# Performance work log

Measured on AMD Instinct MI355X. Metric: run time of the kernel, lower is better.

Reference implementation:

```python
import jax, jax.numpy as jnp
import numpy as np

EMA_BETA = 0.9
NUM_HEADS = 16

def causal_prefix_ema(x, beta):
    # x: [b, t, d]; s_t = beta*s_{t-1} + (1-beta)*x_t, s_{-1}=0
    def step(s, xt):
        s = beta * s + (1.0 - beta) * xt
        return s, s
    s0 = jnp.zeros_like(x[:, 0, :])
    _, ys = jax.lax.scan(step, s0, jnp.swapaxes(x, 0, 1))  # [t, b, d]
    return jnp.swapaxes(ys, 0, 1)

def setup_inputs() -> dict:
    key = jax.random.key(0)
    ks = jax.random.split(key, 9)
    b, t, d = 2, 1024, 2048
    sc = lambda fan_in: 1.0 / np.sqrt(fan_in)
    return {
        "x": jax.random.normal(ks[0], (b, t, d), jnp.float32),
        "l3_memory": jax.random.normal(ks[1], (b, 1, d), jnp.float32),
        "wq": jax.random.normal(ks[2], (d, d), jnp.float32) * sc(d),
        "wk": jax.random.normal(ks[3], (d, d), jnp.float32) * sc(d),
        "wv": jax.random.normal(ks[4], (d, d), jnp.float32) * sc(d),
        "wo": jax.random.normal(ks[5], (d, d), jnp.float32) * sc(d),
        "rw1": jax.random.normal(ks[6], (d // 2, d), jnp.float32) * sc(d),
        "rb1": jnp.zeros((d // 2,), jnp.float32),
        "rw2": jax.random.normal(ks[7], (3, d // 2), jnp.float32) * sc(d // 2),
        "rb2": jnp.zeros((3,), jnp.float32),
    }

def reference(x, l3_memory, wq, wk, wv, wo, rw1, rb1, rw2, rb2):
    b, t, d = x.shape
    h = NUM_HEADS
    dh = d // h
    scale = 1.0 / np.sqrt(dh)

    q = x @ wq.T                                   # [b,t,d]
    l1 = x
    l2 = causal_prefix_ema(x, EMA_BETA)            # [b,t,d]
    l3 = jnp.broadcast_to(l3_memory, (b, t, d))    # repeat retrieval memory to length t

    # router: MLP(Q) -> softmax over 3 levels
    hdn = jax.nn.silu(q @ rw1.T + rb1)
    lam = jax.nn.softmax(hdn @ rw2.T + rb2, axis=-1)  # [b,t,3]

    fused = lam[..., 0:1] * l1 + lam[..., 1:2] * l2 + lam[..., 2:3] * l3

    def heads(y):
        return jnp.swapaxes(y.reshape(b, t, h, dh), 1, 2)  # [b,h,t,dh]

    qh = heads(q)
    kh = heads(fused @ wk.T)
    vh = heads(fused @ wv.T)

    scores = jnp.einsum("bhqd,bhkd->bhqk", qh, kh) * scale
    causal = jnp.tril(jnp.ones((t, t), bool))
    scores = jnp.where(causal, scores, jnp.finfo(scores.dtype).min)
    attn = jax.nn.softmax(scores, axis=-1)
    out = jnp.einsum("bhqk,bhkd->bhqd", attn, vh)

    out = jnp.swapaxes(out, 1, 2).reshape(b, t, d) @ wo.T
    return (out, kh, vh, lam)
```

## Files before the change

### kernel.cpp

```cpp
#include <hip/hip_runtime.h>
#include <hip/hip_bf16.h>
#include <math.h>

#define B_  2
#define T_  1024
#define D_  2048
#define H_  16
#define DH_ 128
#define M_  2048
#define DR_ 1024

typedef __attribute__((ext_vector_type(8))) short short8;
typedef __attribute__((ext_vector_type(4))) short sh4;
typedef __attribute__((ext_vector_type(4))) float f32x4;

__device__ __forceinline__ void gld16(const __hip_bfloat16* g, __hip_bfloat16* l) {
  __builtin_amdgcn_global_load_lds(
      (const __attribute__((address_space(1))) unsigned int*)g,
      (__attribute__((address_space(3))) unsigned int*)l, 16, 0, 0);
}

template<int BM, int CMODE, bool SILU>
__global__ __launch_bounds__(256)
void gemm_mfma(const __hip_bfloat16* __restrict__ A,
               const __hip_bfloat16* __restrict__ Bm,
               const float* __restrict__ bias,
               float* __restrict__ C, __hip_bfloat16* __restrict__ Cb,
               float* __restrict__ C2, __hip_bfloat16* __restrict__ Cb2,
               int M, int N, int K)
{
  constexpr int NI = BM / 32;
  constexpr int AC = BM / 64;
  __shared__ __hip_bfloat16 As[2][2][BM * 32];
  __shared__ __hip_bfloat16 Bs[2][2][128 * 32];
  const int tid  = threadIdx.x;
  const int wave = tid >> 6;
  const int lane = tid & 63;
  const int m0 = blockIdx.y * BM;
  const int n0 = blockIdx.x * 128;
  const int wm = (wave >> 1) * (BM / 2);
  const int wn = (wave & 1) * 64;

  const int srow = lane >> 2;
  const int scol = (lane & 3) * 8;
  const __hip_bfloat16* Ag = A  + (size_t)(m0 + wave * (BM / 4) + srow) * K + scol;
  const __hip_bfloat16* Bg = Bm + (size_t)(n0 + wave * 32 + srow) * K + scol;

  const int fr = lane & 15;
  const int fk = (lane >> 4) * 8;

  f32x4 acc[NI][4];
  #pragma unroll
  for (int i = 0; i < NI; ++i)
    #pragma unroll
    for (int j = 0; j < 4; ++j) acc[i][j] = (f32x4)0.f;

  auto stage = [&](int bf, int k0) {
    #pragma unroll
    for (int h = 0; h < 2; ++h) {
      #pragma unroll
      for (int c = 0; c < AC; ++c)
        gld16(Ag + k0 + h * 32 + (size_t)(c * 16) * K,
              &As[bf][h][(wave * (BM / 4) + c * 16) * 32]);
      #pragma unroll
      for (int c = 0; c < 2; ++c)
        gld16(Bg + k0 + h * 32 + (size_t)(c * 16) * K,
              &Bs[bf][h][(wave * 32 + c * 16) * 32]);
    }
  };

  stage(0, 0);
  __syncthreads();
  int cur = 0;
  for (int k0 = 0; k0 < K; k0 += 64) {
    if (k0 + 64 < K) stage(cur ^ 1, k0 + 64);
    #pragma unroll
    for (int h = 0; h < 2; ++h) {
      short8 af[NI], bfr[4];
      #pragma unroll
      for (int i = 0; i < NI; ++i)
        af[i]  = *(const short8*)&As[cur][h][(wm + i * 16 + fr) * 32 + fk];
      #pragma unroll
      for (int j = 0; j < 4; ++j)
        bfr[j] = *(const short8*)&Bs[cur][h][(wn + j * 16 + fr) * 32 + fk];
      #pragma unroll
      for (int i = 0; i < NI; ++i)
        #pragma unroll
        for (int j = 0; j < 4; ++j)
          acc[i][j] = __builtin_amdgcn_mfma_f32_16x16x32_bf16(af[i], bfr[j], acc[i][j], 0, 0, 0);
    }
    __syncthreads();
    cur ^= 1;
  }

  #pragma unroll
  for (int i = 0; i < NI; ++i) {
    #pragma unroll
    for (int j = 0; j < 4; ++j) {
      const int row0 = m0 + wm + i * 16 + (lane >> 4) * 4;
      const int col  = n0 + wn + j * 16 + (lane & 15);
      float vr[4];
      #pragma unroll
      for (int r = 0; r < 4; ++r) {
        float v = acc[i][j][r];
        if (bias) v += bias[col];
        if (SILU) v = v / (1.f + __expf(-v));
        vr[r] = v;
      }
      if (CMODE == 0) {
        #pragma unroll
        for (int r = 0; r < 4; ++r) C[(size_t)(row0 + r) * N + col] = vr[r];
      } else if (CMODE == 1) {
        #pragma unroll
        for (int r = 0; r < 4; ++r) Cb[(size_t)(row0 + r) * N + col] = __float2bfloat16(vr[r]);
      } else {
        const int bb = row0 >> 10, t0v = row0 & 1023;
        if (col < D_) {
          const int hh = col >> 7, dd = col & 127;
          #pragma unroll
          for (int r = 0; r < 4; ++r) {
            const size_t idx = (((size_t)(bb * H_ + hh)) * T_ + t0v + r) * DH_ + dd;
            C[idx] = vr[r];
            Cb[idx] = __float2bfloat16(vr[r]);
          }
        } else {
          const int c2 = col - D_;
          const int hh = c2 >> 7, dd = c2 & 127;
          #pragma unroll
          for (int r = 0; r < 4; ++r)
            C2[(((size_t)(bb * H_ + hh)) * T_ + t0v + r) * DH_ + dd] = vr[r];
          __hip_bfloat16 tmp[4];
          #pragma unroll
          for (int r = 0; r < 4; ++r) tmp[r] = __float2bfloat16(vr[r]);
          *(sh4*)(Cb2 + (((size_t)(bb * H_ + hh)) * DH_ + dd) * T_ + t0v) = *(const sh4*)tmp;
        }
      }
    }
  }
}

__global__ __launch_bounds__(256)
void cvt6(const float* __restrict__ s0, const float* __restrict__ s1,
          const float* __restrict__ s2, const float* __restrict__ s3,
          const float* __restrict__ s4, const float* __restrict__ s5,
          __hip_bfloat16* d0, __hip_bfloat16* d1, __hip_bfloat16* d2,
          __hip_bfloat16* d3, __hip_bfloat16* d4, __hip_bfloat16* d5,
          int n0, int n1, int n2, int n3, int n4, int n5)
{
  const float* s; __hip_bfloat16* d; int n;
  switch (blockIdx.y) {
    case 0: s = s0; d = d0; n = n0; break;
    case 1: s = s1; d = d1; n = n1; break;
    case 2: s = s2; d = d2; n = n2; break;
    case 3: s = s3; d = d3; n = n3; break;
    case 4: s = s4; d = d4; n = n4; break;
    default: s = s5; d = d5; n = n5; break;
  }
  const int i = (blockIdx.x * 256 + threadIdx.x) * 4;
  if (i < n) {
    float4 v = *(const float4*)(s + i);
    d[i + 0] = __float2bfloat16(v.x);
    d[i + 1] = __float2bfloat16(v.y);
    d[i + 2] = __float2bfloat16(v.z);
    d[i + 3] = __float2bfloat16(v.w);
  }
}

__global__ __launch_bounds__(256)
void ema_scan(const float* __restrict__ x, float* __restrict__ l2)
{
  const int b  = blockIdx.z;
  const int t0 = blockIdx.y * 64;
  const int d  = blockIdx.x * 256 + threadIdx.x;
  const float* xp = x  + (size_t)b * T_ * D_ + d;
  float*       lp = l2 + (size_t)b * T_ * D_ + d;
  float s = 0.f;
  #pragma unroll 4
  for (int t = t0; t < t0 + 64; ++t) {
    s = 0.9f * s + 0.1f * xp[(size_t)t * D_];
    lp[(size_t)t * D_] = s;
  }
}

__global__ __launch_bounds__(256)
void ema_carry(const float* __restrict__ l2loc, float* __restrict__ carry)
{
  const int i = blockIdx.x * 256 + threadIdx.x;
  const int b = i >> 11, d = i & 2047;
  const float A = 1.1790184577738583e-3f;
  float c = 0.f;
  carry[((size_t)b * 16 + 0) * D_ + d] = 0.f;
  for (int ch = 1; ch < 16; ++ch) {
    const float lf = l2loc[((size_t)b * T_ + ch * 64 - 1) * D_ + d];
    c = lf + A * c;
    carry[((size_t)b * 16 + ch) * D_ + d] = c;
  }
}

__global__ __launch_bounds__(256)
void router_kernel(const float* __restrict__ hdn, const float* __restrict__ rw2,
                   const float* __restrict__ rb2, float* __restrict__ lam)
{
  const int lane = threadIdx.x & 63;
  const int w    = threadIdx.x >> 6;
  const int m    = blockIdx.x * 4 + w;
  const float* hp = hdn + (size_t)m * DR_;
  float s0 = 0.f, s1 = 0.f, s2 = 0.f;
  for (int k = lane * 4; k < DR_; k += 256) {
    float4 h4 = *(const float4*)(hp + k);
    float4 w0 = *(const float4*)(rw2 + k);
    float4 w1 = *(const float4*)(rw2 + DR_ + k);
    float4 w2 = *(const float4*)(rw2 + 2 * DR_ + k);
    s0 += h4.x * w0.x + h4.y * w0.y + h4.z * w0.z + h4.w * w0.w;
    s1 += h4.x * w1.x + h4.y * w1.y + h4.z * w1.z + h4.w * w1.w;
    s2 += h4.x * w2.x + h4.y * w2.y + h4.z * w2.z + h4.w * w2.w;
  }
  #pragma unroll
  for (int off = 32; off > 0; off >>= 1) {
    s0 += __shfl_down(s0, off);
    s1 += __shfl_down(s1, off);
    s2 += __shfl_down(s2, off);
  }
  if (lane == 0) {
    s0 += rb2[0]; s1 += rb2[1]; s2 += rb2[2];
    float mx = fmaxf(s0, fmaxf(s1, s2));
    float e0 = __expf(s0 - mx), e1 = __expf(s1 - mx), e2 = __expf(s2 - mx);
    float inv = 1.f / (e0 + e1 + e2);
    lam[(size_t)m * 3 + 0] = e0 * inv;
    lam[(size_t)m * 3 + 1] = e1 * inv;
    lam[(size_t)m * 3 + 2] = e2 * inv;
  }
}

__global__ __launch_bounds__(256)
void fuse_bf16(const float* __restrict__ x, const float* __restrict__ l2,
               const float* __restrict__ l3m, const float* __restrict__ lam,
               const float* __restrict__ carry, __hip_bfloat16* __restrict__ fb)
{
  const int i4 = blockIdx.x * 256 + threadIdx.x;
  const int m  = i4 >> 9;
  const int c  = (i4 & 511) << 2;
  const int b  = m >> 10;
  const int t  = m & 1023;
  const int ch = t >> 6, off = t & 63;
  const float p = __expf((float)(off + 1) * -0.105360515657f);
  const float w0 = lam[m * 3 + 0], w1 = lam[m * 3 + 1], w2 = lam[m * 3 + 2];
  const float4 xv = *(const float4*)(x   + (size_t)m * D_ + c);
  const float4 ev = *(const float4*)(l2  + (size_t)m * D_ + c);
  const float4 gv = *(const float4*)(l3m + (size_t)b * D_ + c);
  const float4 cv = *(const float4*)(carry + ((size_t)b * 16 + ch) * D_ + c);
  __hip_bfloat16* o = fb + (size_t)m * D_ + c;
  o[0] = __float2bfloat16(w0 * xv.x + w1 * (ev.x + p * cv.x) + w2 * gv.x);
  o[1] = __float2bfloat16(w0 * xv.y + w1 * (ev.y + p * cv.y) + w2 * gv.y);
  o[2] = __float2bfloat16(w0 * xv.z + w1 * (ev.z + p * cv.z) + w2 * gv.z);
  o[3] = __float2bfloat16(w0 * xv.w + w1 * (ev.w + p * cv.w) + w2 * gv.w);
}

__global__ __launch_bounds__(256)
void flash_mfma(const __hip_bfloat16* __restrict__ qg,
                const __hip_bfloat16* __restrict__ kg,
                const __hip_bfloat16* __restrict__ vg,
                __hip_bfloat16* __restrict__ og)
{
  __shared__ __hip_bfloat16 Ks[64 * 136];
  __shared__ __hip_bfloat16 Vt[128 * 72];
  __shared__ __hip_bfloat16 Ps[64 * 72];
  const int tid  = threadIdx.x;
  const int wave = tid >> 6, lane = tid & 63;
  const int L    = blockIdx.x;
  const int halfg = L >> 8, idx = L & 255;
  const int bh = (idx >> 4) | (halfg << 4);
  const int qt = halfg ? (15 - (idx & 15)) : (idx & 15);
  const int b = bh >> 4, h = bh & 15;
  const int q0 = qt * 64;
  const int lo = lane & 15, hi = lane >> 4;

  short8 aq[4];
  {
    const __hip_bfloat16* qsrc = qg + (size_t)(b * T_ + q0 + wave * 16 + lo) * D_ + h * DH_;
    #pragma unroll
    for (int kk = 0; kk < 4; ++kk)
      aq[kk] = *(const short8*)(qsrc + kk * 32 + hi * 8);
  }

  f32x4 oacc[8];
  #pragma unroll
  for (int i = 0; i < 8; ++i) oacc[i] = (f32x4)0.f;
  float mrow[4] = {-INFINITY, -INFINITY, -INFINITY, -INFINITY};
  float lrow[4] = {0.f, 0.f, 0.f, 0.f};

  const __hip_bfloat16* kbp = kg + (size_t)bh * T_ * DH_;
  const __hip_bfloat16* vbp = vg + (size_t)bh * DH_ * T_;
  const float scale = 0.08838834764831845f;

  short8 kreg[4], vreg[4];
  auto load_tile = [&](int k0) {
    #pragma unroll
    for (int i = 0; i < 4; ++i) {
      const int ci = tid + 256 * i;
      const int r = ci >> 4, j = ci & 15;
      kreg[i] = *(const short8*)(kbp + (size_t)(k0 + r) * DH_ + j * 8);
      const int dd = ci >> 3, j2 = ci & 7;
      vreg[i] = *(const short8*)(vbp + (size_t)dd * T_ + k0 + j2 * 8);
    }
  };

  load_tile(0);
  for (int kt = 0; kt <= qt; ++kt) {
    #pragma unroll
    for (int i = 0; i < 4; ++i) {
      const int ci = tid + 256 * i;
      const int r = ci >> 4, j = ci & 15;
      *(short8*)&Ks[r * 136 + j * 8] = kreg[i];
      const int dd = ci >> 3, j2 = ci & 7;
      *(short8*)&Vt[dd * 72 + j2 * 8] = vreg[i];
    }
    __syncthreads();
    if (kt < qt) load_tile((kt + 1) * 64);

    f32x4 sc[4];
    __builtin_amdgcn_s_setprio(1);
    #pragma unroll
    for (int nt = 0; nt < 4; ++nt) {
      sc[nt] = (f32x4)0.f;
      #pragma unroll
      for (int kk = 0; kk < 4; ++kk) {
        short8 bk = *(const short8*)&Ks[(nt * 16 + lo) * 136 + kk * 32 + hi * 8];
        sc[nt] = __builtin_amdgcn_mfma_f32_16x16x32_bf16(aq[kk], bk, sc[nt], 0, 0, 0);
      }
    }
    __builtin_amdgcn_s_setprio(0);
    #pragma unroll
    for (int nt = 0; nt < 4; ++nt)
      #pragma unroll
      for (int r = 0; r < 4; ++r) sc[nt][r] *= scale;
    if (kt == qt) {
      const int qrow = q0 + wave * 16 + hi * 4;
      #pragma unroll
      for (int nt = 0; nt < 4; ++nt) {
        const int key = qt * 64 + nt * 16 + lo;
        #pragma unroll
        for (int r = 0; r < 4; ++r)
          if (key > qrow + r) sc[nt][r] = -1e30f;
      }
    }
    float alpha[4];
    #pragma unroll
    for (int r = 0; r < 4; ++r) {
      float mx = fmaxf(fmaxf(sc[0][r], sc[1][r]), fmaxf(sc[2][r], sc[3][r]));
      mx = fmaxf(mx, __shfl_xor(mx, 1));
      mx = fmaxf(mx, __shfl_xor(mx, 2));
      mx = fmaxf(mx, __shfl_xor(mx, 4));
      mx = fmaxf(mx, __shfl_xor(mx, 8));
      const float nm = fmaxf(mrow[r], mx);
      alpha[r] = __expf(mrow[r] - nm);
      mrow[r] = nm;
      float ls = 0.f;
      #pragma unroll
      for (int nt = 0; nt < 4; ++nt) {
        float p = __expf(sc[nt][r] - nm);
        sc[nt][r] = p;
        ls += p;
      }
      ls += __shfl_xor(ls, 1);
      ls += __shfl_xor(ls, 2);
      ls += __shfl_xor(ls, 4);
      ls += __shfl_xor(ls, 8);
      lrow[r] = lrow[r] * alpha[r] + ls;
    }
    #pragma unroll
    for (int nt = 0; nt < 4; ++nt)
      #pragma unroll
      for (int r = 0; r < 4; ++r)
        Ps[(wave * 16 + hi * 4 + r) * 72 + nt * 16 + lo] = __float2bfloat16(sc[nt][r]);
    #pragma unroll
    for (int n2 = 0; n2 < 8; ++n2)
      #pragma unroll
      for (int r = 0; r < 4; ++r) oacc[n2][r] *= alpha[r];
    short8 ap[2];
    #pragma unroll
    for (int k2 = 0; k2 < 2; ++k2)
      ap[k2] = *(const short8*)&Ps[(wave * 16 + lo) * 72 + k2 * 32 + hi * 8];
    __builtin_amdgcn_s_setprio(1);
    #pragma unroll
    for (int n2 = 0; n2 < 8; ++n2) {
      #pragma unroll
      for (int k2 = 0; k2 < 2; ++k2) {
        short8 bv = *(const short8*)&Vt[(n2 * 16 + lo) * 72 + k2 * 32 + hi * 8];
        oacc[n2] = __builtin_amdgcn_mfma_f32_16x16x32_bf16(ap[k2], bv, oacc[n2], 0, 0, 0);
      }
    }
    __builtin_amdgcn_s_setprio(0);
    __syncthreads();
  }

  float inv[4];
  #pragma unroll
  for (int r = 0; r < 4; ++r) inv[r] = 1.f / lrow[r];
  __hip_bfloat16* od = og + (size_t)(b * T_ + q0 + wave * 16 + hi * 4) * D_ + h * DH_;
  #pragma unroll
  for (int n2 = 0; n2 < 8; ++n2)
    #pragma unroll
    for (int r = 0; r < 4; ++r)
      od[(size_t)r * D_ + n2 * 16 + lo] = __float2bfloat16(oacc[n2][r] * inv[r]);
}

extern "C" void kernel_launch(void* const* d_in, const int* in_sizes, int n_in,
                              void* d_out, int out_size, void* d_ws, size_t ws_size,
                              hipStream_t stream)
{
  const float* x   = (const float*)d_in[0];
  const float* l3m = (const float*)d_in[1];
  const float* wq  = (const float*)d_in[2];
  const float* wk  = (const float*)d_in[3];
  const float* wv  = (const float*)d_in[4];
  const float* wo  = (const float*)d_in[5];
  const float* rw1 = (const float*)d_in[6];
  const float* rb1 = (const float*)d_in[7];
  const float* rw2 = (const float*)d_in[8];
  const float* rb2 = (const float*)d_in[9];

  float* out = (float*)d_out;
  float* kh  = out + 4194304;
  float* vh  = out + 8388608;
  float* lam = out + 12582912;

  char* wsb = (char*)d_ws;
  float*          l2_f32 = (float*)(wsb);
  float*          hdn    = (float*)(wsb + (16u << 20));
  __hip_bfloat16* wkb    = (__hip_bfloat16*)(wsb + (24u << 20));
  __hip_bfloat16* wvb    = (__hip_bfloat16*)(wsb + (32u << 20));
  __hip_bfloat16* wob    = (__hip_bfloat16*)(wsb + (40u << 20));
  __hip_bfloat16* fusedb = (__hip_bfloat16*)(wsb + (48u << 20));
  __hip_bfloat16* attnb  = (__hip_bfloat16*)(wsb + (56u << 20));
  __hip_bfloat16* khb    = (__hip_bfloat16*)(wsb + (64u << 20));
  __hip_bfloat16* vtb    = (__hip_bfloat16*)(wsb + (72u << 20));
  float*          carry  = (float*)attnb;
  __hip_bfloat16* wqb  = (__hip_bfloat16*)kh;
  __hip_bfloat16* rw1b = (__hip_bfloat16*)kh + 4194304;
  __hip_bfloat16* xb   = (__hip_bfloat16*)vh;
  __hip_bfloat16* qb   = (__hip_bfloat16*)out;

  dim3 blk(256);

  cvt6<<<dim3(4096, 6), blk, 0, stream>>>(x, wq, wk, wv, wo, rw1,
                                          xb, wqb, wkb, wvb, wob, rw1b,
                                          M_ * D_, D_ * D_, D_ * D_, D_ * D_, D_ * D_, DR_ * D_);
  ema_scan<<<dim3(8, 16, 2), blk, 0, stream>>>(x, l2_f32);
  ema_carry<<<dim3(16), blk, 0, stream>>>(l2_f32, carry);
  gemm_mfma<64, 1, false><<<dim3(16, 32), blk, 0, stream>>>(xb, wqb, nullptr, nullptr, qb, nullptr, nullptr, M_, D_, D_);
  gemm_mfma<64, 0, true><<<dim3(8, 32), blk, 0, stream>>>(qb, rw1b, rb1, hdn, nullptr, nullptr, nullptr, M_, DR_, D_);
  router_kernel<<<dim3(512), blk, 0, stream>>>(hdn, rw2, rb2, lam);
  fuse_bf16<<<dim3(4096), blk, 0, stream>>>(x, l2_f32, l3m, lam, carry, fusedb);
  gemm_mfma<128, 4, false><<<dim3(32, 16), blk, 0, stream>>>(fusedb, wkb, nullptr, kh, khb, vh, vtb, M_, 2 * D_, D_);
  flash_mfma<<<dim3(512), blk, 0, stream>>>(qb, khb, vtb, attnb);
  gemm_mfma<64, 0, false><<<dim3(16, 32), blk, 0, stream>>>(attnb, wob, nullptr, out, nullptr, nullptr, nullptr, M_, D_, D_);
}
```

Measured before the change: 345.9 us.

## Use 4-stage LDS ring with explicit vmcnt waits in GEMM mainloop

Replaces the double-buffered 64-wide K step with a 4-buffer ring of 32-wide K tiles, prefetching three tiles ahead. Explicit s_waitcnt vmcnt counts and a raw s_barrier replace __syncthreads, so in-flight global-to-LDS loads can overlap MFMA work. It also raises wave priority around the MFMA block. The hand-coded vmcnt values depend on the exact number of loads issued per stage, and one barrier per iteration with the ring spacing relies on subtle reuse safety.

Measured after the change: 366.8 us. +6.1%, slower.

```diff
diff --git a/kernel.cpp b/kernel.cpp
--- a/kernel.cpp
+++ b/kernel.cpp
@@ -20,6 +20,8 @@
       (__attribute__((address_space(3))) unsigned int*)l, 16, 0, 0);
 }
 
+#define WAITV(n) asm volatile("s_waitcnt vmcnt(" #n ")" ::: "memory")
+
 template<int BM, int CMODE, bool SILU>
 __global__ __launch_bounds__(256)
 void gemm_mfma(const __hip_bfloat16* __restrict__ A,
@@ -31,8 +33,8 @@
 {
   constexpr int NI = BM / 32;
   constexpr int AC = BM / 64;
-  __shared__ __hip_bfloat16 As[2][2][BM * 32];
-  __shared__ __hip_bfloat16 Bs[2][2][128 * 32];
+  __shared__ __hip_bfloat16 As[4][BM * 32];
+  __shared__ __hip_bfloat16 Bs[4][128 * 32];
   const int tid  = threadIdx.x;
   const int wave = tid >> 6;
   const int lane = tid & 63;
@@ -57,40 +59,50 @@
 
   auto stage = [&](int bf, int k0) {
     #pragma unroll
-    for (int h = 0; h < 2; ++h) {
-      #pragma unroll
-      for (int c = 0; c < AC; ++c)
-        gld16(Ag + k0 + h * 32 + (size_t)(c * 16) * K,
-              &As[bf][h][(wave * (BM / 4) + c * 16) * 32]);
-      #pragma unroll
-      for (int c = 0; c < 2; ++c)
-        gld16(Bg + k0 + h * 32 + (size_t)(c * 16) * K,
-              &Bs[bf][h][(wave * 32 + c * 16) * 32]);
-    }
+    for (int c = 0; c < AC; ++c)
+      gld16(Ag + k0 + (size_t)(c * 16) * K,
+            &As[bf][(wave * (BM / 4) + c * 16) * 32]);
+    #pragma unroll
+    for (int c = 0; c < 2; ++c)
+      gld16(Bg + k0 + (size_t)(c * 16) * K,
+            &Bs[bf][(wave * 32 + c * 16) * 32]);
   };
 
+  const int NT = K >> 5;
   stage(0, 0);
-  __syncthreads();
-  int cur = 0;
-  for (int k0 = 0; k0 < K; k0 += 64) {
-    if (k0 + 64 < K) stage(cur ^ 1, k0 + 64);
-    #pragma unroll
-    for (int h = 0; h < 2; ++h) {
-      short8 af[NI], bfr[4];
-      #pragma unroll
-      for (int i = 0; i < NI; ++i)
-        af[i]  = *(const short8*)&As[cur][h][(wm + i * 16 + fr) * 32 + fk];
+  stage(1, 32);
+  stage(2, 64);
+  int bufc = 0;
+  for (int t = 0; t < NT; ++t) {
+    if constexpr (BM == 128) {
+      if (t <= NT - 3)      WAITV(8);
+      else if (t == NT - 2) WAITV(4);
+      else                  WAITV(0);
+    } else {
+      if (t <= NT - 3)      WAITV(6);
+      else if (t == NT - 2) WAITV(3);
+      else                  WAITV(0);
+    }
+    __builtin_amdgcn_s_barrier();
+    if (t + 3 < NT) {
+      int b3 = bufc + 3; if (b3 >= 4) b3 -= 4;
+      stage(b3, (t + 3) * 32);
+    }
+    short8 af[NI], bfr[4];
+    #pragma unroll
+    for (int i = 0; i < NI; ++i)
+      af[i]  = *(const short8*)&As[bufc][(wm + i * 16 + fr) * 32 + fk];
+    #pragma unroll
+    for (int j = 0; j < 4; ++j)
+      bfr[j] = *(const short8*)&Bs[bufc][(wn + j * 16 + fr) * 32 + fk];
+    __builtin_amdgcn_s_setprio(1);
+    #pragma unroll
+    for (int i = 0; i < NI; ++i)
       #pragma unroll
       for (int j = 0; j < 4; ++j)
-        bfr[j] = *(const short8*)&Bs[cur][h][(wn + j * 16 + fr) * 32 + fk];
-      #pragma unroll
-      for (int i = 0; i < NI; ++i)
-        #pragma unroll
-        for (int j = 0; j < 4; ++j)
-          acc[i][j] = __builtin_amdgcn_mfma_f32_16x16x32_bf16(af[i], bfr[j], acc[i][j], 0, 0, 0);
-    }
-    __syncthreads();
-    cur ^= 1;
+        acc[i][j] = __builtin_amdgcn_mfma_f32_16x16x32_bf16(af[i], bfr[j], acc[i][j], 0, 0, 0);
+    __builtin_amdgcn_s_setprio(0);
+    bufc = (bufc == 3) ? 0 : bufc + 1;
   }
 
   #pragma unroll
```
